# Optimization experiments

Measured on AMD Instinct MI355X. Metric: run time of the kernel, lower is better.

The kernel has to match this reference:

```python
import jax, jax.numpy as jnp
import numpy as np

N_HEADS = 32
N_KV_HEADS = 8
HEAD_DIM = 64
D_MODEL = 2048
SLIDING_WINDOW = 512
ROPE_THETA = 10000.0
PAST_LENGTH = 0
EPS = 1e-6


def setup_inputs() -> dict:
    key = jax.random.key(0)
    k1, k2, k3 = jax.random.split(key, 3)
    B, S = 1, 2048
    q_size = N_HEADS * HEAD_DIM
    kv_size = N_KV_HEADS * HEAD_DIM
    return {
        "x": jax.random.normal(k1, (B, S, D_MODEL), dtype=jnp.float32),
        "w_qkv": jax.random.normal(k2, (q_size + 2 * kv_size, D_MODEL), dtype=jnp.float32) * (D_MODEL ** -0.5),
        "w_out": jax.random.normal(k3, (D_MODEL, q_size), dtype=jnp.float32) * (q_size ** -0.5),
        "q_norm_w": jnp.ones((HEAD_DIM,), dtype=jnp.float32),
        "k_norm_w": jnp.ones((HEAD_DIM,), dtype=jnp.float32),
    }


def _rms_norm(x, w):
    xf = x.astype(jnp.float32)
    rms = jax.lax.rsqrt(jnp.mean(xf * xf, axis=-1, keepdims=True) + EPS)
    return (xf * rms).astype(x.dtype) * w


def _rope(q, k, past_length):
    # q: [b, h, s, d], k: [b, kv, s, d]
    s, d = q.shape[2], q.shape[3]
    inv_freq = 1.0 / (ROPE_THETA ** (jnp.arange(0, d, 2, dtype=jnp.float32) / d))
    pos = jnp.arange(s, dtype=jnp.float32) + past_length
    ang = pos[:, None] * inv_freq[None, :]            # [s, d/2]
    emb = jnp.concatenate([ang, ang], axis=-1)        # [s, d]
    cos, sin = jnp.cos(emb), jnp.sin(emb)

    def rot_half(x):
        x1, x2 = jnp.split(x, 2, axis=-1)
        return jnp.concatenate([-x2, x1], axis=-1)

    q = q * cos + rot_half(q) * sin
    k = k * cos + rot_half(k) * sin
    return q, k


def _sliding_mask(seq_len, total_len, past_length):
    q_idx = jnp.arange(seq_len)[:, None]
    k_idx = jnp.arange(total_len)[None, :]
    causal = (q_idx + past_length) >= k_idx
    window = (q_idx + past_length - k_idx) < SLIDING_WINDOW
    keep = causal & window
    return jnp.where(keep, 0.0, -jnp.inf).astype(jnp.float32)[None, None]


def reference(x, w_qkv, w_out, q_norm_w, k_norm_w):
    b, s, _ = x.shape
    n_rep = N_HEADS // N_KV_HEADS
    q_size = N_HEADS * HEAD_DIM
    kv_size = N_KV_HEADS * HEAD_DIM

    qkv = jnp.einsum('bsd,od->bso', x, w_qkv)
    q, k, v = jnp.split(qkv, [q_size, q_size + kv_size], axis=-1)
    q = q.reshape(b, s, N_HEADS, HEAD_DIM).transpose(0, 2, 1, 3)
    k = k.reshape(b, s, N_KV_HEADS, HEAD_DIM).transpose(0, 2, 1, 3)
    v = v.reshape(b, s, N_KV_HEADS, HEAD_DIM).transpose(0, 2, 1, 3)

    q = _rms_norm(q, q_norm_w)
    k = _rms_norm(k, k_norm_w)
    q, k = _rope(q, k, PAST_LENGTH)

    k_rep = jnp.repeat(k, n_rep, axis=1)  # [b, H, s, d]
    v_rep = jnp.repeat(v, n_rep, axis=1)

    scale = HEAD_DIM ** -0.5
    scores = jnp.einsum('bhqd,bhkd->bhqk', q, k_rep) * scale
    scores = scores + _sliding_mask(s, s, PAST_LENGTH)
    probs = jax.nn.softmax(scores, axis=-1)
    attn = jnp.einsum('bhqk,bhkd->bhqd', probs, v_rep)

    attn = attn.transpose(0, 2, 1, 3).reshape(b, s, q_size)
    return jnp.einsum('bso,do->bsd', attn, w_out)
```

## Files before the change

### kernel.cpp

```cpp
#include <hip/hip_runtime.h>

typedef unsigned short u16;
typedef unsigned int u32;
typedef __bf16 bf16x8 __attribute__((ext_vector_type(8)));
typedef float f32x4 __attribute__((ext_vector_type(4)));
typedef float f32x16 __attribute__((ext_vector_type(16)));
typedef u16 u16x8 __attribute__((ext_vector_type(8)));
typedef u32 u32x2 __attribute__((ext_vector_type(2)));
typedef u32 u32x4 __attribute__((ext_vector_type(4)));

#define MFMA16(a, b, c) __builtin_amdgcn_mfma_f32_16x16x32_bf16((a), (b), (c), 0, 0, 0)
#define MFMA32(a, b, c) __builtin_amdgcn_mfma_f32_32x32x16_bf16((a), (b), (c), 0, 0, 0)

__device__ __forceinline__ u16 f2bf(float f) {
    unsigned int u = __float_as_uint(f);
    u = (u + 0x7FFF + ((u >> 16) & 1)) >> 16;
    return (u16)u;
}

__device__ __forceinline__ float bf2f(u16 v) {
    return __uint_as_float(((u32)v) << 16);
}

__device__ __forceinline__ u32 cvtpk(float a, float b) {
    u32 d;
    asm("v_cvt_pk_bf16_f32 %0, %1, %2" : "=v"(d) : "v"(a), "v"(b));
    return d;
}

__device__ __forceinline__ void gld_lds16(const u16* g, u16* l) {
    __builtin_amdgcn_global_load_lds(
        (const __attribute__((address_space(1))) unsigned int*)g,
        (__attribute__((address_space(3))) unsigned int*)l, 16, 0, 0);
}

__global__ __launch_bounds__(256) void cvt_bf16(const float* __restrict__ in,
                                                u16* __restrict__ out, int n4) {
    int idx = blockIdx.x * blockDim.x + threadIdx.x;
    int stride = gridDim.x * blockDim.x;
    for (int i = idx; i < n4; i += stride) {
        float4 v = reinterpret_cast<const float4*>(in)[i];
        ushort4 o;
        o.x = f2bf(v.x); o.y = f2bf(v.y); o.z = f2bf(v.z); o.w = f2bf(v.w);
        reinterpret_cast<ushort4*>(out)[i] = o;
    }
}

__global__ __launch_bounds__(256) void reduce_add(const float4* __restrict__ a,
                                                  const float4* __restrict__ b,
                                                  float4* __restrict__ o, int n4) {
    int idx = blockIdx.x * blockDim.x + threadIdx.x;
    int stride = gridDim.x * blockDim.x;
    for (int i = idx; i < n4; i += stride) {
        float4 va = a[i], vb = b[i];
        float4 vo = {va.x + vb.x, va.y + vb.y, va.z + vb.z, va.w + vb.w};
        o[i] = vo;
    }
}

template <int SPLITK, int RM, int RN, int XN, bool OBF16>
__global__ __launch_bounds__(512) void gemm_bt(const u16* __restrict__ A,
                                               const u16* __restrict__ B,
                                               void* __restrict__ Cv,
                                               int M, int N, int K) {
    __shared__ __align__(16) u16 As[3][128 * 32];
    __shared__ __align__(16) u16 Bs[3][256 * 32];

    int bid = blockIdx.x;
    int xcd = bid & 7;
    int r = bid >> 3;
    int tm = (xcd / XN) * RM + (r / RN);
    int tn = (xcd % XN) * RN + (r % RN);
    int m0 = tm << 7, n0 = tn << 8;

    int Ks = K / SPLITK;
    int kbase = blockIdx.y * Ks;

    int t = threadIdx.x;
    int w = t >> 6, l = t & 63, lrow = l & 15, lhi = l >> 4;
    int wr = w >> 2, wc = w & 3;

    int rowA = t >> 2;
    int col0 = (((t & 3) ^ ((t >> 3) & 3)) << 3);

    const u16* Ag = A + (size_t)m0 * K + kbase;
    const u16* Bg = B + (size_t)n0 * K + kbase;

    auto stage = [&](int sbuf, int kt) {
        int k0 = kt << 5;
        gld_lds16(Ag + (size_t)rowA * K + k0 + col0, &As[sbuf][t * 8]);
        gld_lds16(Bg + (size_t)rowA * K + k0 + col0, &Bs[sbuf][t * 8]);
        gld_lds16(Bg + (size_t)(rowA + 128) * K + k0 + col0, &Bs[sbuf][t * 8 + 4096]);
    };

    f32x4 acc[4][4] = {};
    int NT = Ks >> 5;
    stage(0, 0); stage(1, 1); stage(2, 2);
    asm volatile("s_waitcnt vmcnt(6)" ::: "memory");
    asm volatile("s_barrier" ::: "memory");
    int cur = 0;
    for (int kt = 0; kt < NT; ++kt) {
        bf16x8 af[4], bfr[4];
#pragma unroll
        for (int i = 0; i < 4; ++i) {
            int row = wr * 64 + i * 16 + lrow;
            af[i] = *(const bf16x8*)&As[cur][row * 32 + ((lhi ^ ((row >> 1) & 3)) << 3)];
        }
#pragma unroll
        for (int j = 0; j < 4; ++j) {
            int row = wc * 64 + j * 16 + lrow;
            bfr[j] = *(const bf16x8*)&Bs[cur][row * 32 + ((lhi ^ ((row >> 1) & 3)) << 3)];
        }
        asm volatile("s_waitcnt lgkmcnt(0)" ::: "memory");
        __builtin_amdgcn_sched_barrier(0);
        asm volatile("s_barrier" ::: "memory");
        if (kt + 3 < NT) stage(cur, kt + 3);
#pragma unroll
        for (int i = 0; i < 4; ++i)
#pragma unroll
            for (int j = 0; j < 4; ++j)
                acc[i][j] = MFMA16(af[i], bfr[j], acc[i][j]);
        if (kt + 1 < NT) {
            if (kt + 3 < NT)      asm volatile("s_waitcnt vmcnt(6)" ::: "memory");
            else if (kt + 2 < NT) asm volatile("s_waitcnt vmcnt(3)" ::: "memory");
            else                  asm volatile("s_waitcnt vmcnt(0)" ::: "memory");
            asm volatile("s_barrier" ::: "memory");
        }
        cur = (cur == 2) ? 0 : cur + 1;
    }
#pragma unroll
    for (int i = 0; i < 4; ++i) {
#pragma unroll
        for (int j = 0; j < 4; ++j) {
            int crow = m0 + wr * 64 + i * 16 + lhi * 4;
            int ccol = n0 + wc * 64 + j * 16 + lrow;
            if (OBF16) {
                u16* cp = (u16*)Cv + (size_t)blockIdx.y * ((size_t)M * N)
                                   + (size_t)crow * N + ccol;
#pragma unroll
                for (int r2 = 0; r2 < 4; ++r2) cp[(size_t)r2 * N] = f2bf(acc[i][j][r2]);
            } else {
                float* cp = (float*)Cv + (size_t)blockIdx.y * ((size_t)M * N)
                                       + (size_t)crow * N + ccol;
#pragma unroll
                for (int r2 = 0; r2 < 4; ++r2) cp[(size_t)r2 * N] = acc[i][j][r2];
            }
        }
    }
}

__global__ __launch_bounds__(256) void qkv_post(const u16* __restrict__ qkv0,
                                                const u16* __restrict__ qkv1,
                                                const float* __restrict__ qw,
                                                const float* __restrict__ kw,
                                                u16* __restrict__ qb,
                                                u16* __restrict__ kb,
                                                u16* __restrict__ vb) {
    const float C = 0.18033688011112042f;
    int s = blockIdx.x;
    int t = threadIdx.x, w = t >> 6, lane = t & 63;
    const u16* row0 = qkv0 + (size_t)s * 3072;
    const u16* row1 = qkv1 + (size_t)s * 3072;
    int d2 = lane & 31;
    float inv = exp2f(-(float)d2 * (13.287712379549449f / 32.0f));
    float ang = (float)s * inv;
    float cs = cosf(ang), sn = sinf(ang);
    for (int h = w; h < 48; h += 4) {
        float v = bf2f(row0[h * 64 + lane]) + bf2f(row1[h * 64 + lane]);
        if (h < 40) {
            float ss = v * v;
#pragma unroll
            for (int m = 32; m; m >>= 1) ss += __shfl_xor(ss, m);
            float rms = rsqrtf(ss * (1.0f / 64.0f) + 1e-6f);
            float wgt = (h < 32) ? qw[lane] : kw[lane];
            v = v * rms * wgt;
            float part = __shfl_xor(v, 32);
            float rot = (lane < 32) ? -part : part;
            v = v * cs + rot * sn;
            if (h < 32)
                qb[((size_t)h * 2048 + s) * 64 + lane] = f2bf(v * C);
            else
                kb[((size_t)(h - 32) * 2048 + s) * 64 + lane] = f2bf(v);
        } else {
            vb[((size_t)(h - 40) * 2048 + s) * 64 + lane] = f2bf(v);
        }
    }
}

__global__ __launch_bounds__(256) void transpose_v(const u16* __restrict__ vb,
                                                   u16* __restrict__ vt) {
    int kv = blockIdx.y;
    int s0 = blockIdx.x * 256;
    __shared__ __align__(16) u16 tile[64][256];
    int t = threadIdx.x;
    int sl = t >> 3;
    int d0 = (t & 7) * 8;
#pragma unroll
    for (int j = 0; j < 8; ++j) {
        int s = sl + j * 32;
        u16x8 v = *(const u16x8*)(vb + ((size_t)kv * 2048 + s0 + s) * 64 + d0);
#pragma unroll
        for (int e = 0; e < 8; ++e) tile[d0 + e][s] = v[e];
    }
    __syncthreads();
    int d = t >> 2;
    int so = (t & 3) * 64;
#pragma unroll
    for (int j = 0; j < 8; ++j) {
        int s_local = so + j * 8;
        *(u16x8*)(vt + ((size_t)kv * 64 + d) * 2048 + s0 + s_local) =
            *(const u16x8*)&tile[d][s_local];
    }
}

__global__ __launch_bounds__(256) void attn_fa7(const u16* __restrict__ qb,
                                                const u16* __restrict__ kb,
                                                const u16* __restrict__ vt,
                                                u16* __restrict__ ab) {
    int qt = blockIdx.x, h = blockIdx.y, kv = h >> 2;
    int t = threadIdx.x, w = t >> 6, l = t & 63;
    int lq = l & 31, hi = l >> 5;
    int qlo_blk = qt * 128;
    int qlo = qlo_blk + w * 32;
    __shared__ __align__(16) u16 Kt[2][32 * 64];
    __shared__ __align__(16) u16 Vt[2][64 * 32];
    __shared__ u16 sm[4][32][66];

    const u16* qrow = qb + ((size_t)h * 2048 + qlo + lq) * 64 + hi * 8;
    bf16x8 qf[4];
#pragma unroll
    for (int dk = 0; dk < 4; ++dk) qf[dk] = *(const bf16x8*)(qrow + dk * 16);

    f32x16 oa = {}, ob = {};
    float lsum = 0.f;

    int ktA = (qlo_blk >= 512) ? ((qlo_blk >> 5) - 16) : 0;
    int ktB = (qlo_blk >> 5) + 3;
    const u16* kb_h = kb + (size_t)kv * 2048 * 64;
    const u16* vt_h = vt + (size_t)kv * 64 * 2048;

    int sk_row = t >> 3, sk_c = ((t & 7) ^ (sk_row & 7)) << 3;
    int sv_row = t >> 2, sv_c = (((t & 3) ^ ((t >> 3) & 3))) << 3;

    auto stage = [&](int buf, int kt) {
        int k0 = kt << 5;
        gld_lds16(kb_h + (size_t)(k0 + sk_row) * 64 + sk_c, &Kt[buf][t * 8]);
        gld_lds16(vt_h + (size_t)sv_row * 2048 + k0 + sv_c, &Vt[buf][t * 8]);
    };

    stage(0, ktA);
    int cur = 0;
    for (int kt = ktA; kt <= ktB; ++kt) {
        if (kt < ktB) {
            stage(cur ^ 1, kt + 1);
            asm volatile("s_waitcnt vmcnt(2)" ::: "memory");
        } else {
            asm volatile("s_waitcnt vmcnt(0)" ::: "memory");
        }
        asm volatile("s_barrier" ::: "memory");

        int k0 = kt << 5;
        bool active = (k0 <= qlo + 31) && (k0 >= qlo - 542);
        if (active) {
            bf16x8 kf[4], vaf[2], vbf[2];
#pragma unroll
            for (int c = 0; c < 4; ++c)
                kf[c] = *(const bf16x8*)&Kt[cur][lq * 64 + (((c * 2 + hi) ^ (lq & 7)) << 3)];
#pragma unroll
            for (int vi = 0; vi < 2; ++vi) {
                int swz = ((vi * 2 + hi) ^ ((lq >> 1) & 3)) << 3;
                vaf[vi] = *(const bf16x8*)&Vt[cur][lq * 32 + swz];
                vbf[vi] = *(const bf16x8*)&Vt[cur][(lq + 32) * 32 + swz];
            }
            asm volatile("s_waitcnt lgkmcnt(0)" ::: "memory");
            __builtin_amdgcn_sched_barrier(0);

            f32x16 s = {};
            s = MFMA32(kf[0], qf[0], s);
            s = MFMA32(kf[1], qf[1], s);
            s = MFMA32(kf[2], qf[2], s);
            s = MFMA32(kf[3], qf[3], s);

            bool edge = (k0 + 31 > qlo) || (qlo + 31 - k0 >= 512);
            if (edge) {
                int q = qlo + lq;
#pragma unroll
                for (int r = 0; r < 16; ++r) {
                    int k = k0 + (r & 3) + 8 * (r >> 2) + 4 * hi;
                    if (!((unsigned)(q - k) < 512u)) s[r] = -1e30f;
                }
            }
            float p[16];
#pragma unroll
            for (int r = 0; r < 16; ++r) {
                p[r] = exp2f(s[r]);
                lsum += p[r];
            }
            u32 pk0 = cvtpk(p[0], p[1]),   pk1 = cvtpk(p[2], p[3]);
            u32 pk2 = cvtpk(p[4], p[5]),   pk3 = cvtpk(p[6], p[7]);
            u32 pk4 = cvtpk(p[8], p[9]),   pk5 = cvtpk(p[10], p[11]);
            u32 pk6 = cvtpk(p[12], p[13]), pk7 = cvtpk(p[14], p[15]);
            u32x2 r02 = __builtin_amdgcn_permlane32_swap(pk0, pk2, false, false);
            u32x2 r13 = __builtin_amdgcn_permlane32_swap(pk1, pk3, false, false);
            u32x2 r46 = __builtin_amdgcn_permlane32_swap(pk4, pk6, false, false);
            u32x2 r57 = __builtin_amdgcn_permlane32_swap(pk5, pk7, false, false);
            bf16x8 b0, b1;
            {
                u32* bp = (u32*)&b0;
                bp[0] = r02[0]; bp[1] = r13[0]; bp[2] = r02[1]; bp[3] = r13[1];
                u32* bq = (u32*)&b1;
                bq[0] = r46[0]; bq[1] = r57[0]; bq[2] = r46[1]; bq[3] = r57[1];
            }
            oa = MFMA32(vaf[0], b0, oa);
            oa = MFMA32(vaf[1], b1, oa);
            ob = MFMA32(vbf[0], b0, ob);
            ob = MFMA32(vbf[1], b1, ob);
        }
        asm volatile("s_barrier" ::: "memory");
        cur ^= 1;
    }

    lsum += __shfl_xor(lsum, 32);
    float inv = 1.0f / lsum;
#pragma unroll
    for (int rp = 0; rp < 8; ++rp) {
        int r = rp * 2;
        int d = (r & 3) + 8 * (r >> 2) + 4 * hi;
        *(u32*)&sm[w][lq][d]      = cvtpk(oa[r] * inv, oa[r + 1] * inv);
        *(u32*)&sm[w][lq][d + 32] = cvtpk(ob[r] * inv, ob[r + 1] * inv);
    }
    asm volatile("s_waitcnt lgkmcnt(0)" ::: "memory");
    int qr = l >> 1, dbase = (l & 1) * 32;
    size_t orow = (size_t)(qlo + qr) * 2048 + h * 64 + dbase;
#pragma unroll
    for (int c2 = 0; c2 < 8; ++c2) {
        u32 w0 = *(const u32*)&sm[w][qr][dbase + c2 * 4];
        u32 w1 = *(const u32*)&sm[w][qr][dbase + c2 * 4 + 2];
        u32x2 val = { w0, w1 };
        *(u32x2*)(ab + orow + c2 * 4) = val;
    }
}

extern "C" void kernel_launch(void* const* d_in, const int* in_sizes, int n_in,
                              void* d_out, int out_size, void* d_ws, size_t ws_size,
                              hipStream_t stream) {
    const float* x     = (const float*)d_in[0];
    const float* w_qkv = (const float*)d_in[1];
    const float* w_out = (const float*)d_in[2];
    const float* qw    = (const float*)d_in[3];
    const float* kw    = (const float*)d_in[4];
    float* out = (float*)d_out;

    char* ws = (char*)d_ws;
    u16*   x_b    = (u16*)(ws);
    u16*   wB     = (u16*)(ws + 8388608);
    u16*   q_b    = (u16*)(ws);
    u16*   k_b    = (u16*)(ws + 8388608);
    u16*   v_b    = (u16*)(ws + 10485760);
    u16*   v_t    = (u16*)(ws + 12582912);
    u16*   P0     = (u16*)(ws + 20971520);
    float* O0     = (float*)(ws + 20971520);
    float* O1     = (float*)(ws + 37748736);
    u16*   attn_b = (u16*)(ws + 54525952);

    cvt_bf16<<<2048, 256, 0, stream>>>(x, x_b, 2048 * 2048 / 4);
    cvt_bf16<<<2048, 256, 0, stream>>>(w_qkv, wB, 3072 * 2048 / 4);
    gemm_bt<2, 8, 3, 4, true><<<dim3(192, 2), 512, 0, stream>>>(
        x_b, wB, P0, 2048, 3072, 2048);
    qkv_post<<<2048, 256, 0, stream>>>(P0, P0 + (size_t)2048 * 3072, qw, kw,
                                       q_b, k_b, v_b);
    transpose_v<<<dim3(8, 8), 256, 0, stream>>>(v_b, v_t);
    attn_fa7<<<dim3(16, 32), 256, 0, stream>>>(q_b, k_b, v_t, attn_b);
    cvt_bf16<<<2048, 256, 0, stream>>>(w_out, wB, 2048 * 2048 / 4);
    gemm_bt<2, 4, 4, 2, false><<<dim3(128, 2), 512, 0, stream>>>(
        attn_b, wB, O0, 2048, 2048, 2048);
    reduce_add<<<1024, 256, 0, stream>>>((const float4*)O0, (const float4*)O1,
                                         (float4*)out, 2048 * 2048 / 4);
}
```

Baseline: 142.9 us.

## Merge input conversions, fold w_out conversion into attention grid, widen KV tiles

The two fp32-to-bf16 conversions of x and w_qkv become a single launch. The w_out conversion moves into 128 extra blocks of the attention kernel, writing to a separate buffer so it can overlap with attention work. The attention kernel now stages 64-key tiles instead of 32, which halves the number of barrier and pipeline iterations, at the cost of more LDS and more registers held across the QK and PV phases.

Result: faster. 129.0 us (-9.7%).

```diff
diff --git a/kernel.cpp b/kernel.cpp
--- a/kernel.cpp
+++ b/kernel.cpp
@@ -34,15 +34,23 @@
         (__attribute__((address_space(3))) unsigned int*)l, 16, 0, 0);
 }
 
-__global__ __launch_bounds__(256) void cvt_bf16(const float* __restrict__ in,
-                                                u16* __restrict__ out, int n4) {
+__global__ __launch_bounds__(256) void cvt2_bf16(const float* __restrict__ in1,
+                                                 u16* __restrict__ out1, int n41,
+                                                 const float* __restrict__ in2,
+                                                 u16* __restrict__ out2, int n42) {
     int idx = blockIdx.x * blockDim.x + threadIdx.x;
     int stride = gridDim.x * blockDim.x;
-    for (int i = idx; i < n4; i += stride) {
-        float4 v = reinterpret_cast<const float4*>(in)[i];
+    for (int i = idx; i < n41; i += stride) {
+        float4 v = reinterpret_cast<const float4*>(in1)[i];
         ushort4 o;
         o.x = f2bf(v.x); o.y = f2bf(v.y); o.z = f2bf(v.z); o.w = f2bf(v.w);
-        reinterpret_cast<ushort4*>(out)[i] = o;
+        reinterpret_cast<ushort4*>(out1)[i] = o;
+    }
+    for (int i = idx; i < n42; i += stride) {
+        float4 v = reinterpret_cast<const float4*>(in2)[i];
+        ushort4 o;
+        o.x = f2bf(v.x); o.y = f2bf(v.y); o.z = f2bf(v.z); o.w = f2bf(v.w);
+        reinterpret_cast<ushort4*>(out2)[i] = o;
     }
 }
 
@@ -213,17 +221,31 @@
     }
 }
 
-__global__ __launch_bounds__(256) void attn_fa7(const u16* __restrict__ qb,
+__global__ __launch_bounds__(256) void attn_fa8(const u16* __restrict__ qb,
                                                 const u16* __restrict__ kb,
                                                 const u16* __restrict__ vt,
-                                                u16* __restrict__ ab) {
-    int qt = blockIdx.x, h = blockIdx.y, kv = h >> 2;
+                                                u16* __restrict__ ab,
+                                                const float* __restrict__ wout,
+                                                u16* __restrict__ wb2) {
+    int bid = blockIdx.x;
+    if (bid >= 512) {
+        int idx = (bid - 512) * 256 + threadIdx.x;
+        int stride = 128 * 256;
+        for (int i = idx; i < 2048 * 2048 / 4; i += stride) {
+            float4 v = reinterpret_cast<const float4*>(wout)[i];
+            ushort4 o;
+            o.x = f2bf(v.x); o.y = f2bf(v.y); o.z = f2bf(v.z); o.w = f2bf(v.w);
+            reinterpret_cast<ushort4*>(wb2)[i] = o;
+        }
+        return;
+    }
+    int qt = bid & 15, h = bid >> 4, kv = h >> 2;
     int t = threadIdx.x, w = t >> 6, l = t & 63;
     int lq = l & 31, hi = l >> 5;
     int qlo_blk = qt * 128;
     int qlo = qlo_blk + w * 32;
-    __shared__ __align__(16) u16 Kt[2][32 * 64];
-    __shared__ __align__(16) u16 Vt[2][64 * 32];
+    __shared__ __align__(16) u16 Kt[2][64 * 64];
+    __shared__ __align__(16) u16 Vt[2][64 * 64];
     __shared__ u16 sm[4][32][66];
 
     const u16* qrow = qb + ((size_t)h * 2048 + qlo + lq) * 64 + hi * 8;
@@ -234,18 +256,22 @@
     f32x16 oa = {}, ob = {};
     float lsum = 0.f;
 
-    int ktA = (qlo_blk >= 512) ? ((qlo_blk >> 5) - 16) : 0;
-    int ktB = (qlo_blk >> 5) + 3;
+    int kstart = qlo_blk - 511; if (kstart < 0) kstart = 0;
+    int ktA = kstart >> 6;
+    int ktB = (qlo_blk + 127) >> 6;
     const u16* kb_h = kb + (size_t)kv * 2048 * 64;
     const u16* vt_h = vt + (size_t)kv * 64 * 2048;
 
-    int sk_row = t >> 3, sk_c = ((t & 7) ^ (sk_row & 7)) << 3;
-    int sv_row = t >> 2, sv_c = (((t & 3) ^ ((t >> 3) & 3))) << 3;
+    int srow = t >> 3;
+    int schk = t & 7;
+    int scol = ((schk ^ (srow & 7)) << 3);
 
     auto stage = [&](int buf, int kt) {
-        int k0 = kt << 5;
-        gld_lds16(kb_h + (size_t)(k0 + sk_row) * 64 + sk_c, &Kt[buf][t * 8]);
-        gld_lds16(vt_h + (size_t)sv_row * 2048 + k0 + sv_c, &Vt[buf][t * 8]);
+        int k0 = kt << 6;
+        gld_lds16(kb_h + (size_t)(k0 + srow) * 64 + scol, &Kt[buf][t * 8]);
+        gld_lds16(kb_h + (size_t)(k0 + srow + 32) * 64 + scol, &Kt[buf][2048 + t * 8]);
+        gld_lds16(vt_h + (size_t)srow * 2048 + k0 + scol, &Vt[buf][t * 8]);
+        gld_lds16(vt_h + (size_t)(srow + 32) * 2048 + k0 + scol, &Vt[buf][2048 + t * 8]);
     };
 
     stage(0, ktA);
@@ -253,68 +279,71 @@
     for (int kt = ktA; kt <= ktB; ++kt) {
         if (kt < ktB) {
             stage(cur ^ 1, kt + 1);
-            asm volatile("s_waitcnt vmcnt(2)" ::: "memory");
+            asm volatile("s_waitcnt vmcnt(4)" ::: "memory");
         } else {
             asm volatile("s_waitcnt vmcnt(0)" ::: "memory");
         }
         asm volatile("s_barrier" ::: "memory");
 
-        int k0 = kt << 5;
-        bool active = (k0 <= qlo + 31) && (k0 >= qlo - 542);
+        int k0 = kt << 6;
+        bool active = (k0 <= qlo + 31) && (k0 >= qlo - 574);
         if (active) {
-            bf16x8 kf[4], vaf[2], vbf[2];
-#pragma unroll
-            for (int c = 0; c < 4; ++c)
-                kf[c] = *(const bf16x8*)&Kt[cur][lq * 64 + (((c * 2 + hi) ^ (lq & 7)) << 3)];
-#pragma unroll
-            for (int vi = 0; vi < 2; ++vi) {
-                int swz = ((vi * 2 + hi) ^ ((lq >> 1) & 3)) << 3;
-                vaf[vi] = *(const bf16x8*)&Vt[cur][lq * 32 + swz];
-                vbf[vi] = *(const bf16x8*)&Vt[cur][(lq + 32) * 32 + swz];
+            int swzk = lq & 7;
+            bf16x8 b[2][2];
+#pragma unroll
+            for (int g = 0; g < 2; ++g) {
+                bf16x8 kf0 = *(const bf16x8*)&Kt[cur][(g * 32 + lq) * 64 + (((0 * 2 + hi) ^ swzk) << 3)];
+                bf16x8 kf1 = *(const bf16x8*)&Kt[cur][(g * 32 + lq) * 64 + (((1 * 2 + hi) ^ swzk) << 3)];
+                bf16x8 kf2 = *(const bf16x8*)&Kt[cur][(g * 32 + lq) * 64 + (((2 * 2 + hi) ^ swzk) << 3)];
+                bf16x8 kf3 = *(const bf16x8*)&Kt[cur][(g * 32 + lq) * 64 + (((3 * 2 + hi) ^ swzk) << 3)];
+                asm volatile("s_waitcnt lgkmcnt(0)" ::: "memory");
+                __builtin_amdgcn_sched_barrier(0);
+                f32x16 s = {};
+                s = MFMA32(kf0, qf[0], s);
+                s = MFMA32(kf1, qf[1], s);
+                s = MFMA32(kf2, qf[2], s);
+                s = MFMA32(kf3, qf[3], s);
+
+                int k0g = k0 + g * 32;
+                bool edge = (k0g + 31 > qlo) || (qlo + 31 - k0g >= 512);
+                if (edge) {
+                    int q = qlo + lq;
+#pragma unroll
+                    for (int r = 0; r < 16; ++r) {
+                        int k = k0g + (r & 3) + 8 * (r >> 2) + 4 * hi;
+                        if (!((unsigned)(q - k) < 512u)) s[r] = -1e30f;
+                    }
+                }
+                float p[16];
+#pragma unroll
+                for (int r = 0; r < 16; ++r) {
+                    p[r] = exp2f(s[r]);
+                    lsum += p[r];
+                }
+                u32 pk0 = cvtpk(p[0], p[1]),   pk1 = cvtpk(p[2], p[3]);
+                u32 pk2 = cvtpk(p[4], p[5]),   pk3 = cvtpk(p[6], p[7]);
+                u32 pk4 = cvtpk(p[8], p[9]),   pk5 = cvtpk(p[10], p[11]);
+                u32 pk6 = cvtpk(p[12], p[13]), pk7 = cvtpk(p[14], p[15]);
+                u32x2 r02 = __builtin_amdgcn_permlane32_swap(pk0, pk2, false, false);
+                u32x2 r13 = __builtin_amdgcn_permlane32_swap(pk1, pk3, false, false);
+                u32x2 r46 = __builtin_amdgcn_permlane32_swap(pk4, pk6, false, false);
+                u32x2 r57 = __builtin_amdgcn_permlane32_swap(pk5, pk7, false, false);
+                u32* bp = (u32*)&b[g][0];
+                bp[0] = r02[0]; bp[1] = r13[0]; bp[2] = r02[1]; bp[3] = r13[1];
+                u32* bq = (u32*)&b[g][1];
+                bq[0] = r46[0]; bq[1] = r57[0]; bq[2] = r46[1]; bq[3] = r57[1];
             }
-            asm volatile("s_waitcnt lgkmcnt(0)" ::: "memory");
-            __builtin_amdgcn_sched_barrier(0);
-
-            f32x16 s = {};
-            s = MFMA32(kf[0], qf[0], s);
-            s = MFMA32(kf[1], qf[1], s);
-            s = MFMA32(kf[2], qf[2], s);
-            s = MFMA32(kf[3], qf[3], s);
-
-            bool edge = (k0 + 31 > qlo) || (qlo + 31 - k0 >= 512);
-            if (edge) {
-                int q = qlo + lq;
-#pragma unroll
-                for (int r = 0; r < 16; ++r) {
-                    int k = k0 + (r & 3) + 8 * (r >> 2) + 4 * hi;
-                    if (!((unsigned)(q - k) < 512u)) s[r] = -1e30f;
+#pragma unroll
+            for (int g = 0; g < 2; ++g) {
+#pragma unroll
+                for (int vi = 0; vi < 2; ++vi) {
+                    int chk = ((g * 4 + vi * 2 + hi) ^ swzk) << 3;
+                    bf16x8 va = *(const bf16x8*)&Vt[cur][lq * 64 + chk];
+                    bf16x8 vb_ = *(const bf16x8*)&Vt[cur][(lq + 32) * 64 + chk];
+                    oa = MFMA32(va, b[g][vi], oa);
+                    ob = MFMA32(vb_, b[g][vi], ob);
                 }
             }
-            float p[16];
-#pragma unroll
-            for (int r = 0; r < 16; ++r) {
-                p[r] = exp2f(s[r]);
-                lsum += p[r];
-            }
-            u32 pk0 = cvtpk(p[0], p[1]),   pk1 = cvtpk(p[2], p[3]);
-            u32 pk2 = cvtpk(p[4], p[5]),   pk3 = cvtpk(p[6], p[7]);
-            u32 pk4 = cvtpk(p[8], p[9]),   pk5 = cvtpk(p[10], p[11]);
-            u32 pk6 = cvtpk(p[12], p[13]), pk7 = cvtpk(p[14], p[15]);
-            u32x2 r02 = __builtin_amdgcn_permlane32_swap(pk0, pk2, false, false);
-            u32x2 r13 = __builtin_amdgcn_permlane32_swap(pk1, pk3, false, false);
-            u32x2 r46 = __builtin_amdgcn_permlane32_swap(pk4, pk6, false, false);
-            u32x2 r57 = __builtin_amdgcn_permlane32_swap(pk5, pk7, false, false);
-            bf16x8 b0, b1;
-            {
-                u32* bp = (u32*)&b0;
-                bp[0] = r02[0]; bp[1] = r13[0]; bp[2] = r02[1]; bp[3] = r13[1];
-                u32* bq = (u32*)&b1;
-                bq[0] = r46[0]; bq[1] = r57[0]; bq[2] = r46[1]; bq[3] = r57[1];
-            }
-            oa = MFMA32(vaf[0], b0, oa);
-            oa = MFMA32(vaf[1], b1, oa);
-            ob = MFMA32(vbf[0], b0, ob);
-            ob = MFMA32(vbf[1], b1, ob);
         }
         asm volatile("s_barrier" ::: "memory");
         cur ^= 1;
@@ -362,18 +391,18 @@
     float* O0     = (float*)(ws + 20971520);
     float* O1     = (float*)(ws + 37748736);
     u16*   attn_b = (u16*)(ws + 54525952);
-
-    cvt_bf16<<<2048, 256, 0, stream>>>(x, x_b, 2048 * 2048 / 4);
-    cvt_bf16<<<2048, 256, 0, stream>>>(w_qkv, wB, 3072 * 2048 / 4);
+    u16*   wB2    = (u16*)(ws + 62914560);
+
+    cvt2_bf16<<<2048, 256, 0, stream>>>(x, x_b, 2048 * 2048 / 4,
+                                        w_qkv, wB, 3072 * 2048 / 4);
     gemm_bt<2, 8, 3, 4, true><<<dim3(192, 2), 512, 0, stream>>>(
         x_b, wB, P0, 2048, 3072, 2048);
     qkv_post<<<2048, 256, 0, stream>>>(P0, P0 + (size_t)2048 * 3072, qw, kw,
                                        q_b, k_b, v_b);
     transpose_v<<<dim3(8, 8), 256, 0, stream>>>(v_b, v_t);
-    attn_fa7<<<dim3(16, 32), 256, 0, stream>>>(q_b, k_b, v_t, attn_b);
-    cvt_bf16<<<2048, 256, 0, stream>>>(w_out, wB, 2048 * 2048 / 4);
+    attn_fa8<<<640, 256, 0, stream>>>(q_b, k_b, v_t, attn_b, w_out, wB2);
     gemm_bt<2, 4, 4, 2, false><<<dim3(128, 2), 512, 0, stream>>>(
-        attn_b, wB, O0, 2048, 2048, 2048);
+        attn_b, wB2, O0, 2048, 2048, 2048);
     reduce_add<<<1024, 256, 0, stream>>>((const float4*)O0, (const float4*)O1,
                                          (float4*)out, 2048 * 2048 / 4);
 }
```
